# Optimization experiments

Measured on AMD Instinct MI355X. Metric: run time of the kernel, lower is better.

## Reference

```python
import jax, jax.numpy as jnp
import numpy as np

HW, B, C, NH, NC, HF, WF = 2500, 2, 256, 8, 6, 64, 176
DFF = 4 * C
EPS = 1e-5

def _layernorm(x, g, b):
    m = x.mean(-1, keepdims=True)
    v = ((x - m) ** 2).mean(-1, keepdims=True)
    return (x - m) / jnp.sqrt(v + EPS) * g + b

def _mha(q, kv, in_w, in_b, ow, ob):
    # q: [L,B,C], kv: [S,B,C] (batch_first=False, torch nn.MultiheadAttention)
    L, Bq, Cq = q.shape
    S = kv.shape[0]
    Dh = Cq // NH
    qp = (q @ in_w[:Cq].T + in_b[:Cq]).reshape(L, Bq, NH, Dh)
    kp = (kv @ in_w[Cq:2 * Cq].T + in_b[Cq:2 * Cq]).reshape(S, Bq, NH, Dh)
    vp = (kv @ in_w[2 * Cq:].T + in_b[2 * Cq:]).reshape(S, Bq, NH, Dh)
    att = jnp.einsum('lbhd,sbhd->bhls', qp, kp) * (1.0 / np.sqrt(Dh))
    att = jax.nn.softmax(att, axis=-1)
    out = jnp.einsum('bhls,sbhd->lbhd', att, vp).reshape(L, Bq, Cq)
    return out @ ow.T + ob

def _grid_sample_zeros(feat, grid):
    # feat: [B,N,C,H,W], grid: [B,N,Q,2] in [-1,1]; bilinear, align_corners=False, zero padding
    Bb, N, Cc, Hf, Wf = feat.shape
    Q = grid.shape[2]
    x = (grid[..., 0] + 1.0) * (Wf / 2.0) - 0.5
    y = (grid[..., 1] + 1.0) * (Hf / 2.0) - 0.5
    x0 = jnp.floor(x); y0 = jnp.floor(y)
    wx = x - x0; wy = y - y0
    x0i = x0.astype(jnp.int32); y0i = y0.astype(jnp.int32)
    ff = feat.reshape(Bb, N, Cc, Hf * Wf)
    def corner(xi, yi, w):
        valid = (xi >= 0) & (xi < Wf) & (yi >= 0) & (yi < Hf)
        idx = jnp.clip(yi, 0, Hf - 1) * Wf + jnp.clip(xi, 0, Wf - 1)  # [B,N,Q]
        g = jnp.take_along_axis(ff, jnp.broadcast_to(idx[:, :, None, :], (Bb, N, Cc, Q)), axis=-1)
        return g * (w * valid)[:, :, None, :]
    return (corner(x0i, y0i, (1.0 - wx) * (1.0 - wy)) + corner(x0i + 1, y0i, wx * (1.0 - wy))
            + corner(x0i, y0i + 1, (1.0 - wx) * wy) + corner(x0i + 1, y0i + 1, wx * wy))

def _forward(bev_queries, prev_bev, image_feat, reference_points, camera_intrinsics, camera_extrinsics,
             in_proj_w, in_proj_b, out_proj_w, out_proj_b, tsa_norm_g, tsa_norm_b,
             sca_w, sca_b, sca_norm_g, sca_norm_b, ffn_w1, ffn_b1, ffn_w2, ffn_b2, ffn_norm_g, ffn_norm_b):
    # TSA (dropout is identity in eval)
    tsa_out = _mha(bev_queries, prev_bev, in_proj_w, in_proj_b, out_proj_w, out_proj_b)
    x = _layernorm(bev_queries + tsa_out, tsa_norm_g, tsa_norm_b)
    # SCA: ego->camera->image projection
    R = camera_extrinsics[:, :, :3, :3]            # [B,N,3,3]
    t = camera_extrinsics[:, :, :3, 3]             # [B,N,3]
    R_e2c = jnp.swapaxes(R, -1, -2)
    t_e2c = -jnp.einsum('bnij,bnj->bni', R_e2c, t)
    pts_cam = jnp.einsum('bnij,qj->bnqi', R_e2c, reference_points) + t_e2c[:, :, None, :]  # [B,N,Q,3]
    pts_img = jnp.einsum('bnij,bnqj->bnqi', camera_intrinsics, pts_cam)
    uv = pts_img[..., :2] / jnp.maximum(pts_img[..., 2:3], 1e-5)
    grid = jnp.stack([2.0 * uv[..., 0] / WF - 1.0, 2.0 * uv[..., 1] / HF - 1.0], axis=-1)  # [B,N,Q,2]
    Bq = bev_queries.shape[1]
    feat_r = image_feat.reshape(Bq, NC, C, HF, WF)
    sampled = _grid_sample_zeros(feat_r, grid).mean(axis=1)   # [B,C,Q]
    sampled = jnp.transpose(sampled, (2, 0, 1))               # [Q,B,C]
    sca_out = sampled @ sca_w.T + sca_b
    x = _layernorm(x + sca_out, sca_norm_g, sca_norm_b)
    # FFN (torch nn.GELU default = exact erf)
    h = jax.nn.gelu(x @ ffn_w1 + ffn_b1, approximate=False)
    ffn_out = h @ ffn_w2 + ffn_b2
    return _layernorm(x + ffn_out, ffn_norm_g, ffn_norm_b)

def setup_inputs():
    key = jax.random.key(0)
    ks = jax.random.split(key, 16)
    f = jnp.float32
    s = 0.02
    return {
        'bev_queries': jax.random.normal(ks[0], (HW, B, C), f),
        'prev_bev': jax.random.normal(ks[1], (HW, B, C), f),
        'image_feat': jax.random.normal(ks[2], (B * NC, C, HF, WF), f),
        'reference_points': jax.random.normal(ks[3], (HW, 3), f) * 20.0,
        'camera_intrinsics': jax.random.normal(ks[4], (B, NC, 3, 3), f),
        'camera_extrinsics': jax.random.normal(ks[5], (B, NC, 4, 4), f),
        'spatial_shapes': jnp.array([[HF, WF]], jnp.int32),
        'in_proj_w': jax.random.normal(ks[6], (3 * C, C), f) * s,
        'in_proj_b': jnp.zeros((3 * C,), f),
        'out_proj_w': jax.random.normal(ks[7], (C, C), f) * s,
        'out_proj_b': jnp.zeros((C,), f),
        'tsa_norm_g': jnp.ones((C,), f), 'tsa_norm_b': jnp.zeros((C,), f),
        'sca_w': jax.random.normal(ks[8], (C, C), f) * s,
        'sca_b': jnp.zeros((C,), f),
        'sca_norm_g': jnp.ones((C,), f), 'sca_norm_b': jnp.zeros((C,), f),
        'ffn_w1': jax.random.normal(ks[9], (C, DFF), f) * s,
        'ffn_b1': jnp.zeros((DFF,), f),
        'ffn_w2': jax.random.normal(ks[10], (DFF, C), f) * s,
        'ffn_b2': jnp.zeros((C,), f),
        'ffn_norm_g': jnp.ones((C,), f), 'ffn_norm_b': jnp.zeros((C,), f),
    }

def reference(bev_queries, prev_bev, image_feat, reference_points, camera_intrinsics, camera_extrinsics,
              in_proj_w, in_proj_b, out_proj_w, out_proj_b, tsa_norm_g, tsa_norm_b,
              sca_w, sca_b, sca_norm_g, sca_norm_b, ffn_w1, ffn_b1, ffn_w2, ffn_b2, ffn_norm_g, ffn_norm_b,
              spatial_shapes):
    return _forward(bev_queries, prev_bev, image_feat, reference_points, camera_intrinsics, camera_extrinsics,
                    in_proj_w, in_proj_b, out_proj_w, out_proj_b, tsa_norm_g, tsa_norm_b,
                    sca_w, sca_b, sca_norm_g, sca_norm_b, ffn_w1, ffn_b1, ffn_w2, ffn_b2, ffn_norm_g, ffn_norm_b)
```

## Files before the change

kernel.cpp:

```cpp
#include <hip/hip_runtime.h>

typedef unsigned short u16;
typedef __attribute__((ext_vector_type(8))) __bf16 bf8_t;
typedef __attribute__((ext_vector_type(4))) float f4_t;

union bf8u { u16 u[8]; bf8_t v; uint4 q; };

__device__ __forceinline__ float bf2f(u16 v) {
  return __uint_as_float(((unsigned int)v) << 16);
}
__device__ __forceinline__ u16 f2bf(float f) {
  unsigned int u = __float_as_uint(f);
  unsigned int r = u + 0x7FFFu + ((u >> 16) & 1u);
  return (u16)(r >> 16);
}
__device__ __forceinline__ float bflo(unsigned int w) { return __uint_as_float(w << 16); }
__device__ __forceinline__ float bfhi(unsigned int w) { return __uint_as_float(w & 0xFFFF0000u); }
__device__ __forceinline__ float ldf1(const void* p, size_t i, int isf32) {
  return isf32 ? ((const float*)p)[i] : bf2f(((const u16*)p)[i]);
}

#define LQ    2500
#define LQP   2560
#define BB    2
#define CC    256
#define NCC   6
#define HFF   64
#define WFF   176
#define DFF   1024
#define MROWS 5000

#define WB_UV   256
#define WB_WQKV 240256
#define WB_WOP  633472
#define WB_WSC  764544
#define WB_WF1  895616
#define WB_WF2  1419904
#define WB_S1   1944192
#define WB_S2   (WB_S1 + 2621440)
#define WB_S3   (WB_S2 + 2621440)
#define WB_VT   (WB_S3 + 2621440)
#define WB_H    WB_S2
#define WB_Y3   (WB_S2 + 10485760)

__global__ void detect_k(const u16* __restrict__ rp, int* __restrict__ flag) {
  int bad = 0;
  for (int i = threadIdx.x; i < 7500; i += 64) {
    float v = bf2f(rp[i]);
    if (!(fabsf(v) < 1e6f)) bad = 1;
  }
  int anybad = __any(bad);
  if (threadIdx.x == 0) flag[0] = anybad ? 1 : 0;
}

struct WDesc {
  const void* src[6];
  u16* dst[6];
  int n[6];
  int mode[6];
  int Kd[6], Nd[6];
};
__global__ __launch_bounds__(256) void cvtw_k(WDesc d, const int* __restrict__ flag) {
  const int df = flag[0];
  const int i = blockIdx.y;
  const int n = d.n[i];
  for (int j = blockIdx.x * 256 + threadIdx.x; j < n; j += gridDim.x * 256) {
    if (d.mode[i] == 2) {
      const int row = j / (LQP - LQ), col = LQ + j % (LQP - LQ);
      d.dst[i][(size_t)row * LQP + col] = 0;
    } else if (d.mode[i] == 1) {
      const int K = d.Kd[i], N = d.Nd[i];
      const int nn = j / K, kk = j - nn * K;
      d.dst[i][j] = f2bf(ldf1(d.src[i], (size_t)kk * N + nn, df));
    } else {
      d.dst[i][j] = f2bf(ldf1(d.src[i], j, df));
    }
  }
}

template<int XRAW, int ACT, int RES, int STORE_T>
__global__ __launch_bounds__(64) void gemm_nl(
    const void* __restrict__ Xv, const u16* __restrict__ W,
    const void* __restrict__ bias, size_t boff,
    const void* __restrict__ resv,
    u16* __restrict__ Y, int M, int N, int K, const int* __restrict__ flag)
{
  const int df = flag[0];
  const int lane = threadIdx.x;
  const int ln15 = lane & 15, l4 = lane >> 4;
  const int m0 = blockIdx.x * 16, n0 = blockIdx.y * 64;
  const int am = min(m0 + ln15, M - 1);

  f4_t acc[4];
#pragma unroll
  for (int nt = 0; nt < 4; ++nt) acc[nt] = (f4_t){0.f, 0.f, 0.f, 0.f};

  for (int k0 = 0; k0 < K; k0 += 32) {
    bf8u a;
    if (XRAW && df) {
      const float* p = (const float*)Xv + (size_t)am * K + k0 + l4 * 8;
      float4 r0 = *(const float4*)p, r1 = *(const float4*)(p + 4);
      a.u[0]=f2bf(r0.x); a.u[1]=f2bf(r0.y); a.u[2]=f2bf(r0.z); a.u[3]=f2bf(r0.w);
      a.u[4]=f2bf(r1.x); a.u[5]=f2bf(r1.y); a.u[6]=f2bf(r1.z); a.u[7]=f2bf(r1.w);
    } else {
      a.q = *(const uint4*)((const u16*)Xv + (size_t)am * K + k0 + l4 * 8);
    }
#pragma unroll
    for (int nt = 0; nt < 4; ++nt) {
      bf8u b;
      b.q = *(const uint4*)&W[(size_t)(n0 + nt * 16 + ln15) * K + k0 + l4 * 8];
      acc[nt] = __builtin_amdgcn_mfma_f32_16x16x32_bf16(a.v, b.v, acc[nt], 0, 0, 0);
    }
  }
#pragma unroll
  for (int nt = 0; nt < 4; ++nt) {
    const int gn = n0 + nt * 16 + ln15;
    const float bv = ldf1(bias, boff + gn, df);
#pragma unroll
    for (int r = 0; r < 4; ++r) {
      const int gm = m0 + l4 * 4 + r;
      if (gm < M) {
        float x = acc[nt][r] + bv;
        if (ACT) x = 0.5f * x * (1.f + erff(x * 0.70710678118654752f));
        if (RES == 1)      x += bf2f(((const u16*)resv)[(size_t)gm * N + gn]);
        else if (RES == 2) x += ldf1(resv, (size_t)gm * N + gn, df);
        if (STORE_T) Y[(size_t)(gn + (gm & 1) * 256) * LQP + (gm >> 1)] = f2bf(x);
        else         Y[(size_t)gm * N + gn] = f2bf(x);
      }
    }
  }
}

__global__ __launch_bounds__(256) void attn_mf(
    const u16* __restrict__ Qw, const u16* __restrict__ Kw,
    const u16* __restrict__ Vt, u16* __restrict__ Ow)
{
  __shared__ __align__(16) u16 sP[4][16 * 72];
  const int t = threadIdx.x;
  const int lane = t & 63, w = t >> 6;
  const int ln15 = lane & 15, l4 = lane >> 4;
  const int q0 = blockIdx.x * 64 + w * 16;
  const int by = blockIdx.y;
  const int b = by >> 3, h = by & 7;
  u16* myP = &sP[w][0];
  const float SCL2E = 0.25505654481f;

  bf8u aq;
  {
    const size_t qaddr = ((size_t)(q0 + ln15) * BB + b) * CC + h * 32 + l4 * 8;
    bf8u qr; qr.q = *(const uint4*)&Qw[qaddr];
#pragma unroll
    for (int i = 0; i < 8; ++i) aq.u[i] = f2bf(bf2f(qr.u[i]) * SCL2E);
  }

  f4_t oacc[2];
  oacc[0] = (f4_t){0.f,0.f,0.f,0.f};
  oacc[1] = (f4_t){0.f,0.f,0.f,0.f};
  float m_r[4] = {-1e30f, -1e30f, -1e30f, -1e30f};
  float l_r[4] = {0.f, 0.f, 0.f, 0.f};

  for (int kt = 0; kt < 40; ++kt) {
    const int kb = kt * 64;
    f4_t sv[4];
#pragma unroll
    for (int nt = 0; nt < 4; ++nt) {
      bf8u bk;
      bk.q = *(const uint4*)&Kw[((size_t)(kb + nt * 16 + ln15) * BB + b) * CC + h * 32 + l4 * 8];
      f4_t z = (f4_t){0.f,0.f,0.f,0.f};
      sv[nt] = __builtin_amdgcn_mfma_f32_16x16x32_bf16(aq.v, bk.v, z, 0, 0, 0);
    }
    float p[4][4];
#pragma unroll
    for (int nt = 0; nt < 4; ++nt) {
      const bool ok = (kb + nt * 16 + ln15) < LQ;
#pragma unroll
      for (int r = 0; r < 4; ++r) p[nt][r] = ok ? sv[nt][r] : -1e30f;
    }
#pragma unroll
    for (int r = 0; r < 4; ++r) {
      float mloc = fmaxf(fmaxf(p[0][r], p[1][r]), fmaxf(p[2][r], p[3][r]));
      mloc = fmaxf(mloc, __shfl_xor(mloc, 1));
      mloc = fmaxf(mloc, __shfl_xor(mloc, 2));
      mloc = fmaxf(mloc, __shfl_xor(mloc, 4));
      mloc = fmaxf(mloc, __shfl_xor(mloc, 8));
      const float mn = fmaxf(m_r[r], mloc);
      const float alpha = __builtin_amdgcn_exp2f(m_r[r] - mn);
      m_r[r] = mn;
      float s = 0.f;
#pragma unroll
      for (int nt = 0; nt < 4; ++nt) {
        const float e = __builtin_amdgcn_exp2f(p[nt][r] - mn);
        p[nt][r] = e; s += e;
      }
      s += __shfl_xor(s, 1);
      s += __shfl_xor(s, 2);
      s += __shfl_xor(s, 4);
      s += __shfl_xor(s, 8);
      l_r[r] = l_r[r] * alpha + s;
      oacc[0][r] *= alpha;
      oacc[1][r] *= alpha;
    }
#pragma unroll
    for (int nt = 0; nt < 4; ++nt)
#pragma unroll
      for (int r = 0; r < 4; ++r)
        myP[(l4 * 4 + r) * 72 + nt * 16 + ln15] = f2bf(p[nt][r]);
#pragma unroll
    for (int ks = 0; ks < 2; ++ks) {
      bf8u ap;
      ap.q = *(const uint4*)&myP[ln15 * 72 + ks * 32 + l4 * 8];
#pragma unroll
      for (int nt = 0; nt < 2; ++nt) {
        bf8u bv;
        bv.q = *(const uint4*)&Vt[(size_t)(by * 32 + nt * 16 + ln15) * LQP + kb + ks * 32 + l4 * 8];
        oacc[nt] = __builtin_amdgcn_mfma_f32_16x16x32_bf16(ap.v, bv.v, oacc[nt], 0, 0, 0);
      }
    }
  }
#pragma unroll
  for (int nt = 0; nt < 2; ++nt)
#pragma unroll
    for (int r = 0; r < 4; ++r) {
      const int q = q0 + l4 * 4 + r;
      if (q < LQ) {
        const float val = oacc[nt][r] / l_r[r];
        Ow[((size_t)q * BB + b) * CC + h * 32 + nt * 16 + ln15] = f2bf(val);
      }
    }
}

template<int TOOUT>
__global__ __launch_bounds__(256) void ln_k(const u16* __restrict__ X,
    const void* __restrict__ g, const void* __restrict__ be,
    void* __restrict__ Yv, int rows, const int* __restrict__ flag)
{
  const int df = flag[0];
  const int lane = threadIdx.x & 63;
  const int row = blockIdx.x * 4 + (threadIdx.x >> 6);
  if (row >= rows) return;
  uint2 raw = *(const uint2*)(X + (size_t)row * CC + lane * 4);
  float vx = bflo(raw.x), vy = bfhi(raw.x), vz = bflo(raw.y), vw = bfhi(raw.y);
  float s = vx + vy + vz + vw;
#pragma unroll
  for (int o = 1; o < 64; o <<= 1) s += __shfl_xor(s, o);
  const float mean = s * 0.00390625f;
  const float dx = vx - mean, dy = vy - mean, dz = vz - mean, dw = vw - mean;
  float sq = dx*dx + dy*dy + dz*dz + dw*dw;
#pragma unroll
  for (int o = 1; o < 64; o <<= 1) sq += __shfl_xor(sq, o);
  const float rstd = rsqrtf(sq * 0.00390625f + 1e-5f);
  const float g0 = ldf1(g, lane*4+0, df), g1 = ldf1(g, lane*4+1, df);
  const float g2 = ldf1(g, lane*4+2, df), g3 = ldf1(g, lane*4+3, df);
  const float b0 = ldf1(be, lane*4+0, df), b1 = ldf1(be, lane*4+1, df);
  const float b2 = ldf1(be, lane*4+2, df), b3 = ldf1(be, lane*4+3, df);
  const float y0 = dx * rstd * g0 + b0;
  const float y1 = dy * rstd * g1 + b1;
  const float y2 = dz * rstd * g2 + b2;
  const float y3 = dw * rstd * g3 + b3;
  if (TOOUT && df) {
    float* yp = (float*)Yv + (size_t)row * CC + lane * 4;
    *(float4*)yp = make_float4(y0, y1, y2, y3);
  } else {
    u16* yp = (u16*)Yv + (size_t)row * CC + lane * 4;
    unsigned int lo = (unsigned int)f2bf(y0) | ((unsigned int)f2bf(y1) << 16);
    unsigned int hi = (unsigned int)f2bf(y2) | ((unsigned int)f2bf(y3) << 16);
    *(uint2*)yp = make_uint2(lo, hi);
  }
}

__global__ __launch_bounds__(256) void uv_k(
    const void* __restrict__ refp, const void* __restrict__ intr,
    const void* __restrict__ extr, float* __restrict__ uv,
    const int* __restrict__ flag)
{
  const int df = flag[0];
  const int idx = blockIdx.x * 256 + threadIdx.x;
  if (idx >= BB * NCC * LQ) return;
  const int bc = idx / LQ;
  const int q = idx - bc * LQ;
  float R[3][3], tv[3], Kc[3][3], p[3];
#pragma unroll
  for (int i = 0; i < 3; ++i) {
#pragma unroll
    for (int j = 0; j < 3; ++j) {
      R[i][j] = ldf1(extr, bc*16 + i*4 + j, df);
      Kc[i][j] = ldf1(intr, bc*9 + i*3 + j, df);
    }
    tv[i] = ldf1(extr, bc*16 + i*4 + 3, df);
  }
#pragma unroll
  for (int j = 0; j < 3; ++j) p[j] = ldf1(refp, q*3 + j, df) - tv[j];
  float pc[3];
#pragma unroll
  for (int i = 0; i < 3; ++i) pc[i] = R[0][i]*p[0] + R[1][i]*p[1] + R[2][i]*p[2];
  float im[3];
#pragma unroll
  for (int i = 0; i < 3; ++i) im[i] = Kc[i][0]*pc[0] + Kc[i][1]*pc[1] + Kc[i][2]*pc[2];
  const float z = fmaxf(im[2], 1e-5f);
  uv[(size_t)idx*2 + 0] = im[0] / z - 0.5f;
  uv[(size_t)idx*2 + 1] = im[1] / z - 0.5f;
}

__global__ __launch_bounds__(256) void samp_k(
    const void* __restrict__ feat, const float* __restrict__ uv,
    u16* __restrict__ S, const int* __restrict__ flag)
{
  const int df = flag[0];
  const int c = blockIdx.x;
  const int b = blockIdx.y / 5;
  const int ch = blockIdx.y % 5;
  const int qend = min((ch + 1) * 500, LQ);
  for (int q = ch * 500 + threadIdx.x; q < qend; q += 256) {
    float acc = 0.f;
#pragma unroll
    for (int cam = 0; cam < NCC; ++cam) {
      const int bc = b * NCC + cam;
      const float x = uv[((size_t)bc * LQ + q) * 2 + 0];
      const float y = uv[((size_t)bc * LQ + q) * 2 + 1];
      const float xf = floorf(x), yf = floorf(y);
      const int x0 = (int)xf, y0 = (int)yf;
      const float wx = x - xf, wy = y - yf;
      const size_t base = ((size_t)bc * CC + c) * (HFF * WFF);
      const bool vx0 = (x0 >= 0) & (x0 < WFF);
      const bool vx1 = (x0 + 1 >= 0) & (x0 + 1 < WFF);
      const bool vy0 = (y0 >= 0) & (y0 < HFF);
      const bool vy1 = (y0 + 1 >= 0) & (y0 + 1 < HFF);
      if (vy0) {
        const size_t rb = base + (size_t)y0 * WFF;
        if (vx0) acc += (1.f - wx) * (1.f - wy) * ldf1(feat, rb + x0, df);
        if (vx1) acc += wx * (1.f - wy) * ldf1(feat, rb + x0 + 1, df);
      }
      if (vy1) {
        const size_t rb = base + (size_t)(y0 + 1) * WFF;
        if (vx0) acc += (1.f - wx) * wy * ldf1(feat, rb + x0, df);
        if (vx1) acc += wx * wy * ldf1(feat, rb + x0 + 1, df);
      }
    }
    S[((size_t)q * BB + b) * CC + c] = f2bf(acc * (1.f / 6.f));
  }
}

extern "C" void kernel_launch(void* const* d_in, const int* in_sizes, int n_in,
                              void* d_out, int out_size, void* d_ws, size_t ws_size,
                              hipStream_t stream) {
  (void)in_sizes; (void)n_in; (void)out_size; (void)ws_size;
  char* base = (char*)d_ws;
  int* flag = (int*)base;
  float* UV = (float*)(base + WB_UV);
  u16* WQKV = (u16*)(base + WB_WQKV);
  u16* WOP  = (u16*)(base + WB_WOP);
  u16* WSC  = (u16*)(base + WB_WSC);
  u16* WF1  = (u16*)(base + WB_WF1);
  u16* WF2  = (u16*)(base + WB_WF2);
  u16* S1 = (u16*)(base + WB_S1);
  u16* S2 = (u16*)(base + WB_S2);
  u16* S3 = (u16*)(base + WB_S3);
  u16* VT = (u16*)(base + WB_VT);
  u16* H  = (u16*)(base + WB_H);
  u16* Y3 = (u16*)(base + WB_Y3);

  detect_k<<<1, 64, 0, stream>>>((const u16*)d_in[3], flag);

  WDesc wd;
  wd.src[0] = d_in[7];  wd.dst[0] = WQKV; wd.n[0] = 196608; wd.mode[0] = 0; wd.Kd[0] = 0;    wd.Nd[0] = 0;
  wd.src[1] = d_in[9];  wd.dst[1] = WOP;  wd.n[1] = 65536;  wd.mode[1] = 0; wd.Kd[1] = 0;    wd.Nd[1] = 0;
  wd.src[2] = d_in[13]; wd.dst[2] = WSC;  wd.n[2] = 65536;  wd.mode[2] = 0; wd.Kd[2] = 0;    wd.Nd[2] = 0;
  wd.src[3] = d_in[17]; wd.dst[3] = WF1;  wd.n[3] = 262144; wd.mode[3] = 1; wd.Kd[3] = 256;  wd.Nd[3] = 1024;
  wd.src[4] = d_in[19]; wd.dst[4] = WF2;  wd.n[4] = 262144; wd.mode[4] = 1; wd.Kd[4] = 1024; wd.Nd[4] = 256;
  wd.src[5] = nullptr;  wd.dst[5] = VT;   wd.n[5] = 512 * (LQP - LQ); wd.mode[5] = 2; wd.Kd[5] = 0; wd.Nd[5] = 0;
  cvtw_k<<<dim3(128, 6), 256, 0, stream>>>(wd, flag);

  uv_k<<<(BB * NCC * LQ + 255) / 256, 256, 0, stream>>>(d_in[3], d_in[4], d_in[5], UV, flag);

  gemm_nl<1,0,0,0><<<dim3(313, 4), 64, 0, stream>>>(d_in[0], WQKV,          d_in[8], 0,   nullptr, S1, MROWS, CC, CC, flag);
  gemm_nl<1,0,0,0><<<dim3(313, 4), 64, 0, stream>>>(d_in[1], WQKV + 65536,  d_in[8], 256, nullptr, S2, MROWS, CC, CC, flag);
  gemm_nl<1,0,0,1><<<dim3(313, 4), 64, 0, stream>>>(d_in[1], WQKV + 131072, d_in[8], 512, nullptr, VT, MROWS, CC, CC, flag);

  attn_mf<<<dim3(40, 16), 256, 0, stream>>>(S1, S2, VT, S3);

  gemm_nl<0,0,2,0><<<dim3(313, 4), 64, 0, stream>>>(S3, WOP, d_in[10], 0, d_in[0], S1, MROWS, CC, CC, flag);
  ln_k<0><<<1250, 256, 0, stream>>>(S1, d_in[11], d_in[12], S2, MROWS, flag);

  samp_k<<<dim3(CC, BB * 5), 256, 0, stream>>>(d_in[2], UV, VT, flag);

  gemm_nl<0,0,1,0><<<dim3(313, 4), 64, 0, stream>>>(VT, WSC, d_in[14], 0, S2, S3, MROWS, CC, CC, flag);
  ln_k<0><<<1250, 256, 0, stream>>>(S3, d_in[15], d_in[16], S1, MROWS, flag);

  gemm_nl<0,1,0,0><<<dim3(313, 16), 64, 0, stream>>>(S1, WF1, d_in[18], 0, nullptr, H,  MROWS, DFF, CC,  flag);
  gemm_nl<0,0,1,0><<<dim3(313, 4),  64, 0, stream>>>(H,  WF2, d_in[20], 0, S1,      Y3, MROWS, CC,  DFF, flag);
  ln_k<1><<<1250, 256, 0, stream>>>(Y3, d_in[21], d_in[22], d_out, MROWS, flag);
}
```

Measured before the change: 564.1 us.

## Split attention keys across waves and template GEMM K dimension

The attention kernel now gives each block 16 queries and splits the 40 key tiles across its 4 waves, ten tiles each. Partial max, sum and output are merged through shared memory at the end, split-K style. This raises the grid from 640 to 2512 blocks for better occupancy, at the cost of reloading each query tile four times and an extra shared-memory reduction. The GEMM K dimension becomes a template parameter with unroll 8, and full key tiles skip the masking branch.

```diff
diff --git a/kernel.cpp b/kernel.cpp
--- a/kernel.cpp
+++ b/kernel.cpp
@@ -78,12 +78,12 @@
   }
 }
 
-template<int XRAW, int ACT, int RES, int STORE_T>
+template<int KTPL, int XRAW, int ACT, int RES, int STORE_T>
 __global__ __launch_bounds__(64) void gemm_nl(
     const void* __restrict__ Xv, const u16* __restrict__ W,
     const void* __restrict__ bias, size_t boff,
     const void* __restrict__ resv,
-    u16* __restrict__ Y, int M, int N, int K, const int* __restrict__ flag)
+    u16* __restrict__ Y, int M, int N, const int* __restrict__ flag)
 {
   const int df = flag[0];
   const int lane = threadIdx.x;
@@ -95,20 +95,21 @@
 #pragma unroll
   for (int nt = 0; nt < 4; ++nt) acc[nt] = (f4_t){0.f, 0.f, 0.f, 0.f};
 
-  for (int k0 = 0; k0 < K; k0 += 32) {
+#pragma unroll 8
+  for (int k0 = 0; k0 < KTPL; k0 += 32) {
     bf8u a;
     if (XRAW && df) {
-      const float* p = (const float*)Xv + (size_t)am * K + k0 + l4 * 8;
+      const float* p = (const float*)Xv + (size_t)am * KTPL + k0 + l4 * 8;
       float4 r0 = *(const float4*)p, r1 = *(const float4*)(p + 4);
       a.u[0]=f2bf(r0.x); a.u[1]=f2bf(r0.y); a.u[2]=f2bf(r0.z); a.u[3]=f2bf(r0.w);
       a.u[4]=f2bf(r1.x); a.u[5]=f2bf(r1.y); a.u[6]=f2bf(r1.z); a.u[7]=f2bf(r1.w);
     } else {
-      a.q = *(const uint4*)((const u16*)Xv + (size_t)am * K + k0 + l4 * 8);
+      a.q = *(const uint4*)((const u16*)Xv + (size_t)am * KTPL + k0 + l4 * 8);
     }
 #pragma unroll
     for (int nt = 0; nt < 4; ++nt) {
       bf8u b;
-      b.q = *(const uint4*)&W[(size_t)(n0 + nt * 16 + ln15) * K + k0 + l4 * 8];
+      b.q = *(const uint4*)&W[(size_t)(n0 + nt * 16 + ln15) * KTPL + k0 + l4 * 8];
       acc[nt] = __builtin_amdgcn_mfma_f32_16x16x32_bf16(a.v, b.v, acc[nt], 0, 0, 0);
     }
   }
@@ -131,15 +132,19 @@
   }
 }
 
+#define TPW 10
 __global__ __launch_bounds__(256) void attn_mf(
     const u16* __restrict__ Qw, const u16* __restrict__ Kw,
     const u16* __restrict__ Vt, u16* __restrict__ Ow)
 {
   __shared__ __align__(16) u16 sP[4][16 * 72];
+  __shared__ float sO[4][16][32];
+  __shared__ float sM[4][16];
+  __shared__ float sL[4][16];
   const int t = threadIdx.x;
   const int lane = t & 63, w = t >> 6;
   const int ln15 = lane & 15, l4 = lane >> 4;
-  const int q0 = blockIdx.x * 64 + w * 16;
+  const int q0 = blockIdx.x * 16;
   const int by = blockIdx.y;
   const int b = by >> 3, h = by & 7;
   u16* myP = &sP[w][0];
@@ -147,8 +152,8 @@
 
   bf8u aq;
   {
-    const size_t qaddr = ((size_t)(q0 + ln15) * BB + b) * CC + h * 32 + l4 * 8;
-    bf8u qr; qr.q = *(const uint4*)&Qw[qaddr];
+    const int qrow = min(q0 + ln15, LQ - 1);
+    bf8u qr; qr.q = *(const uint4*)&Qw[((size_t)qrow * BB + b) * CC + h * 32 + l4 * 8];
 #pragma unroll
     for (int i = 0; i < 8; ++i) aq.u[i] = f2bf(bf2f(qr.u[i]) * SCL2E);
   }
@@ -159,7 +164,7 @@
   float m_r[4] = {-1e30f, -1e30f, -1e30f, -1e30f};
   float l_r[4] = {0.f, 0.f, 0.f, 0.f};
 
-  for (int kt = 0; kt < 40; ++kt) {
+  for (int kt = w * TPW; kt < w * TPW + TPW; ++kt) {
     const int kb = kt * 64;
     f4_t sv[4];
 #pragma unroll
@@ -170,11 +175,18 @@
       sv[nt] = __builtin_amdgcn_mfma_f32_16x16x32_bf16(aq.v, bk.v, z, 0, 0, 0);
     }
     float p[4][4];
-#pragma unroll
-    for (int nt = 0; nt < 4; ++nt) {
-      const bool ok = (kb + nt * 16 + ln15) < LQ;
-#pragma unroll
-      for (int r = 0; r < 4; ++r) p[nt][r] = ok ? sv[nt][r] : -1e30f;
+    if (kb + 64 <= LQ) {
+#pragma unroll
+      for (int nt = 0; nt < 4; ++nt)
+#pragma unroll
+        for (int r = 0; r < 4; ++r) p[nt][r] = sv[nt][r];
+    } else {
+#pragma unroll
+      for (int nt = 0; nt < 4; ++nt) {
+        const bool ok = (kb + nt * 16 + ln15) < LQ;
+#pragma unroll
+        for (int r = 0; r < 4; ++r) p[nt][r] = ok ? sv[nt][r] : -1e30f;
+      }
     }
 #pragma unroll
     for (int r = 0; r < 4; ++r) {
@@ -220,13 +232,28 @@
 #pragma unroll
   for (int nt = 0; nt < 2; ++nt)
 #pragma unroll
-    for (int r = 0; r < 4; ++r) {
-      const int q = q0 + l4 * 4 + r;
-      if (q < LQ) {
-        const float val = oacc[nt][r] / l_r[r];
-        Ow[((size_t)q * BB + b) * CC + h * 32 + nt * 16 + ln15] = f2bf(val);
-      }
-    }
+    for (int r = 0; r < 4; ++r)
+      sO[w][l4 * 4 + r][nt * 16 + ln15] = oacc[nt][r];
+  if (ln15 == 0) {
+#pragma unroll
+    for (int r = 0; r < 4; ++r) { sM[w][l4 * 4 + r] = m_r[r]; sL[w][l4 * 4 + r] = l_r[r]; }
+  }
+  __syncthreads();
+#pragma unroll
+  for (int i = t; i < 512; i += 256) {
+    const int row = i >> 5, col = i & 31;
+    const float M = fmaxf(fmaxf(sM[0][row], sM[1][row]), fmaxf(sM[2][row], sM[3][row]));
+    float l = 0.f, O = 0.f;
+#pragma unroll
+    for (int w4 = 0; w4 < 4; ++w4) {
+      const float sc = __builtin_amdgcn_exp2f(sM[w4][row] - M);
+      l += sc * sL[w4][row];
+      O += sc * sO[w4][row][col];
+    }
+    const int q = q0 + row;
+    if (q < LQ)
+      Ow[((size_t)q * BB + b) * CC + h * 32 + col] = f2bf(O / l);
+  }
 }
 
 template<int TOOUT>
@@ -372,21 +399,21 @@
 
   uv_k<<<(BB * NCC * LQ + 255) / 256, 256, 0, stream>>>(d_in[3], d_in[4], d_in[5], UV, flag);
 
-  gemm_nl<1,0,0,0><<<dim3(313, 4), 64, 0, stream>>>(d_in[0], WQKV,          d_in[8], 0,   nullptr, S1, MROWS, CC, CC, flag);
-  gemm_nl<1,0,0,0><<<dim3(313, 4), 64, 0, stream>>>(d_in[1], WQKV + 65536,  d_in[8], 256, nullptr, S2, MROWS, CC, CC, flag);
-  gemm_nl<1,0,0,1><<<dim3(313, 4), 64, 0, stream>>>(d_in[1], WQKV + 131072, d_in[8], 512, nullptr, VT, MROWS, CC, CC, flag);
-
-  attn_mf<<<dim3(40, 16), 256, 0, stream>>>(S1, S2, VT, S3);
-
-  gemm_nl<0,0,2,0><<<dim3(313, 4), 64, 0, stream>>>(S3, WOP, d_in[10], 0, d_in[0], S1, MROWS, CC, CC, flag);
+  gemm_nl<256,1,0,0,0><<<dim3(313, 4), 64, 0, stream>>>(d_in[0], WQKV,          d_in[8], 0,   nullptr, S1, MROWS, CC, flag);
+  gemm_nl<256,1,0,0,0><<<dim3(313, 4), 64, 0, stream>>>(d_in[1], WQKV + 65536,  d_in[8], 256, nullptr, S2, MROWS, CC, flag);
+  gemm_nl<256,1,0,0,1><<<dim3(313, 4), 64, 0, stream>>>(d_in[1], WQKV + 131072, d_in[8], 512, nullptr, VT, MROWS, CC, flag);
+
+  attn_mf<<<dim3(157, 16), 256, 0, stream>>>(S1, S2, VT, S3);
+
+  gemm_nl<256,0,0,2,0><<<dim3(313, 4), 64, 0, stream>>>(S3, WOP, d_in[10], 0, d_in[0], S1, MROWS, CC, flag);
   ln_k<0><<<1250, 256, 0, stream>>>(S1, d_in[11], d_in[12], S2, MROWS, flag);
 
   samp_k<<<dim3(CC, BB * 5), 256, 0, stream>>>(d_in[2], UV, VT, flag);
 
-  gemm_nl<0,0,1,0><<<dim3(313, 4), 64, 0, stream>>>(VT, WSC, d_in[14], 0, S2, S3, MROWS, CC, CC, flag);
+  gemm_nl<256,0,0,1,0><<<dim3(313, 4), 64, 0, stream>>>(VT, WSC, d_in[14], 0, S2, S3, MROWS, CC, flag);
   ln_k<0><<<1250, 256, 0, stream>>>(S3, d_in[15], d_in[16], S1, MROWS, flag);
 
-  gemm_nl<0,1,0,0><<<dim3(313, 16), 64, 0, stream>>>(S1, WF1, d_in[18], 0, nullptr, H,  MROWS, DFF, CC,  flag);
-  gemm_nl<0,0,1,0><<<dim3(313, 4),  64, 0, stream>>>(H,  WF2, d_in[20], 0, S1,      Y3, MROWS, CC,  DFF, flag);
+  gemm_nl<256,0,1,0,0><<<dim3(313, 16), 64, 0, stream>>>(S1, WF1, d_in[18], 0, nullptr, H,  MROWS, DFF, flag);
+  gemm_nl<1024,0,0,1,0><<<dim3(313, 4),  64, 0, stream>>>(H,  WF2, d_in[20], 0, S1,      Y3, MROWS, CC,  flag);
   ln_k<1><<<1250, 256, 0, stream>>>(Y3, d_in[21], d_in[22], d_out, MROWS, flag);
 }
```

Result: faster. 524.0 us (-7.1%).
